# Kernel tuning notes

Hardware: AMD Instinct MI355X
Metric: run time of the kernel (lower is better)

Reference implementation:

```python
import jax, jax.numpy as jnp
import numpy as np

N = 1_000_000
SIZES = (64, 32, 16)
N_REGIONS = 1000
N_CLUSTERS = 16
N_CELLS = 100_000


def setup_inputs() -> dict:
    key = jax.random.key(0)
    ks = jax.random.split(key, 16)
    inp = {}
    for i, s in enumerate(SIZES):
        inp[f"bincounts_{i}"] = jax.random.randint(ks[i], (N, s), 0, 5, dtype=jnp.int32)
    inp["global_binixs"] = jax.random.randint(ks[3], (N, 3), 0, N_REGIONS, dtype=jnp.int32)
    inp["binixs"] = jax.random.randint(ks[4], (N, 3), 0, 16, dtype=jnp.int32)  # < min(SIZES)
    inp["labels"] = jax.random.randint(ks[5], (N_CELLS,), 0, N_CLUSTERS, dtype=jnp.int32)
    inp["local_cell_ix"] = jax.random.randint(ks[6], (N,), 0, N_CELLS, dtype=jnp.int32)
    for i, s in enumerate(SIZES):
        inp[f"baseline_{i}"] = jax.random.normal(ks[7 + i], (N_REGIONS, s), dtype=jnp.float32)
        inp[f"diff_{i}"] = jax.random.normal(ks[10 + i], (N_CLUSTERS,), dtype=jnp.float32)
    return inp


def reference(bincounts_0, bincounts_1, bincounts_2, global_binixs, binixs,
              labels, local_cell_ix, baseline_0, baseline_1, baseline_2,
              diff_0, diff_1, diff_2):
    # cluster label per fragment (int, constant)
    frag_labels = labels[local_cell_ix]  # [N]
    bincounts = (bincounts_0, bincounts_1, bincounts_2)
    baselines = (baseline_0, baseline_1, baseline_2)
    diffs = (diff_0, diff_1, diff_2)
    logprob = jnp.zeros((bincounts_0.shape[0],), dtype=jnp.float32)
    for i in range(3):
        bc, bw, dw = bincounts[i], baselines[i], diffs[i]
        S = bw.shape[1]
        # fragment_embedding (indicator) * differential scalar + baseline row
        dvals = dw[frag_labels]  # [N]
        uh = (bc > 1).astype(jnp.float32) * dvals[:, None] + bw[global_binixs[:, i]]  # [N, S]
        logh = jax.nn.log_softmax(uh, axis=1) + jnp.log(jnp.float32(S))
        logprob = logprob + jnp.take_along_axis(logh, binixs[:, i:i + 1], axis=1)[:, 0]
    return logprob
```

## Files before the change

kernel.cpp:

```cpp
#include <hip/hip_runtime.h>

#define LOG64f 4.1588830833596715f
#define LOG32f 3.4657359027997265f
#define LOG16f 2.7725887222397810f


__device__ __forceinline__ void expsum4(const int4 c, const float4 w, const float dv,
                                        const int b, const int sub, float& s, float& ub)
{
    const float u0 = (c.x > 1 ? dv : 0.f) + w.x;
    const float u1 = (c.y > 1 ? dv : 0.f) + w.y;
    const float u2 = (c.z > 1 ? dv : 0.f) + w.z;
    const float u3 = (c.w > 1 ? dv : 0.f) + w.w;
    s  = (__expf(u0) + __expf(u1)) + (__expf(u2) + __expf(u3));
    ub = 0.f;
    if (sub == (b >> 2)) {
        const int r = b & 3;
        ub = r == 0 ? u0 : r == 1 ? u1 : r == 2 ? u2 : u3;
    }
}

__device__ __forceinline__ float chunk16(
    const int lane,
    const int4 c00, const int4 c01, const int4 c02, const int4 c03,
    const int4 c10, const int4 c11, const int4 c20,
    const float dva, const float dvb, const float dvc,
    const int g0v, const int g1v, const int g2v,
    const int b0v, const int b1v, const int b2v,
    const float* __restrict__ bw0, const float* __restrict__ bw1,
    const float* __restrict__ bw2)
{
    const int fl = lane & 15;
    const int s16 = lane >> 4, s8 = lane >> 3, s4 = lane >> 2;
    const int f00 = s16, f01 = 4 + s16, f02 = 8 + s16, f03 = 12 + s16;
    const int f10 = s8,  f11 = 8 + s8;
    const int f20 = s4;
    const int sub0 = lane & 15, sub1 = lane & 7, sub2 = lane & 3;

    const float dv00 = __shfl(dva, f00), dv01 = __shfl(dva, f01),
                dv02 = __shfl(dva, f02), dv03 = __shfl(dva, f03);
    const int   g00  = __shfl(g0v, f00), g01  = __shfl(g0v, f01),
                g02  = __shfl(g0v, f02), g03  = __shfl(g0v, f03);
    const int   b00  = __shfl(b0v, f00), b01  = __shfl(b0v, f01),
                b02  = __shfl(b0v, f02), b03  = __shfl(b0v, f03);
    const float dv10 = __shfl(dvb, f10), dv11 = __shfl(dvb, f11);
    const int   g10  = __shfl(g1v, f10), g11  = __shfl(g1v, f11);
    const int   b10  = __shfl(b1v, f10), b11  = __shfl(b1v, f11);
    const float dv20 = __shfl(dvc, f20);
    const int   g20  = __shfl(g2v, f20);
    const int   b20  = __shfl(b2v, f20);

    const float4 w00 = ((const float4*)(bw0 + (size_t)g00 * 64))[sub0];
    const float4 w01 = ((const float4*)(bw0 + (size_t)g01 * 64))[sub0];
    const float4 w02 = ((const float4*)(bw0 + (size_t)g02 * 64))[sub0];
    const float4 w03 = ((const float4*)(bw0 + (size_t)g03 * 64))[sub0];
    const float4 w10 = ((const float4*)(bw1 + (size_t)g10 * 32))[sub1];
    const float4 w11 = ((const float4*)(bw1 + (size_t)g11 * 32))[sub1];
    const float4 w20 = ((const float4*)(bw2 + (size_t)g20 * 16))[sub2];

    float s00, u00, s01, u01, s02, u02, s03, u03;
    expsum4(c00, w00, dv00, b00, sub0, s00, u00);
    expsum4(c01, w01, dv01, b01, sub0, s01, u01);
    expsum4(c02, w02, dv02, b02, sub0, s02, u02);
    expsum4(c03, w03, dv03, b03, sub0, s03, u03);
    #pragma unroll
    for (int off = 1; off <= 8; off <<= 1) {
        s00 += __shfl_xor(s00, off); s01 += __shfl_xor(s01, off);
        s02 += __shfl_xor(s02, off); s03 += __shfl_xor(s03, off);
    }
    float s10, u10, s11, u11;
    expsum4(c10, w10, dv10, b10, sub1, s10, u10);
    expsum4(c11, w11, dv11, b11, sub1, s11, u11);
    #pragma unroll
    for (int off = 1; off <= 4; off <<= 1) {
        s10 += __shfl_xor(s10, off); s11 += __shfl_xor(s11, off);
    }
    float s20, u20;
    expsum4(c20, w20, dv20, b20, sub2, s20, u20);
    s20 += __shfl_xor(s20, 1); s20 += __shfl_xor(s20, 2);

    const int  src0 = (fl & 3) << 4;
    const float m00 = __shfl(s00, src0), m01 = __shfl(s01, src0),
                m02 = __shfl(s02, src0), m03 = __shfl(s03, src0);
    const int j0 = fl >> 2;
    const float S0 = j0 == 0 ? m00 : j0 == 1 ? m01 : j0 == 2 ? m02 : m03;
    const int  h0 = src0 + (b0v >> 2);
    const float x00 = __shfl(u00, h0), x01 = __shfl(u01, h0),
                x02 = __shfl(u02, h0), x03 = __shfl(u03, h0);
    const float U0 = j0 == 0 ? x00 : j0 == 1 ? x01 : j0 == 2 ? x02 : x03;

    const int  src1 = (fl & 7) << 3;
    const float m10 = __shfl(s10, src1), m11 = __shfl(s11, src1);
    const float S1 = (fl >> 3) == 0 ? m10 : m11;
    const int  h1 = src1 + (b1v >> 2);
    const float x10 = __shfl(u10, h1), x11 = __shfl(u11, h1);
    const float U1 = (fl >> 3) == 0 ? x10 : x11;

    const float S2 = __shfl(s20, fl << 2);
    const float U2 = __shfl(u20, (fl << 2) + (b2v >> 2));

    return (U0 - __logf(S0) + LOG64f) +
           (U1 - __logf(S1) + LOG32f) +
           (U2 - __logf(S2) + LOG16f);
}

__global__ __launch_bounds__(256) void frag_pos_dist_kernel(
    const int* __restrict__ bc0, const int* __restrict__ bc1, const int* __restrict__ bc2,
    const int* __restrict__ gix, const int* __restrict__ bix,
    const int* __restrict__ labels, const int* __restrict__ lci,
    const float* __restrict__ bw0, const float* __restrict__ d0,
    const float* __restrict__ bw1, const float* __restrict__ d1,
    const float* __restrict__ bw2, const float* __restrict__ d2,
    float* __restrict__ out, int N)
{
    const int lane = threadIdx.x & 63;
    const int wid  = blockIdx.x * (blockDim.x >> 6) + (threadIdx.x >> 6);
    const int base = wid * 32;
    if (base >= N) return;
    const int fl = lane & 15;
    const int s16 = lane >> 4, s8 = lane >> 3, s4 = lane >> 2;
    const int sub0 = lane & 15, sub1 = lane & 7, sub2 = lane & 3;
    const int NM1 = N - 1;

    const int nA00 = min(base +      s16, NM1), nA01 = min(base +  4 + s16, NM1),
              nA02 = min(base +  8 + s16, NM1), nA03 = min(base + 12 + s16, NM1);
    const int nA10 = min(base +       s8, NM1), nA11 = min(base +  8 +  s8, NM1);
    const int nA20 = min(base +       s4, NM1);
    const int nB00 = min(base + 16 + s16, NM1), nB01 = min(base + 20 + s16, NM1),
              nB02 = min(base + 24 + s16, NM1), nB03 = min(base + 28 + s16, NM1);
    const int nB10 = min(base + 16 +  s8, NM1), nB11 = min(base + 24 +  s8, NM1);
    const int nB20 = min(base + 16 +  s4, NM1);

    const int4 cA00 = ((const int4*)(bc0 + (size_t)nA00 * 64))[sub0];
    const int4 cA01 = ((const int4*)(bc0 + (size_t)nA01 * 64))[sub0];
    const int4 cA02 = ((const int4*)(bc0 + (size_t)nA02 * 64))[sub0];
    const int4 cA03 = ((const int4*)(bc0 + (size_t)nA03 * 64))[sub0];
    const int4 cA10 = ((const int4*)(bc1 + (size_t)nA10 * 32))[sub1];
    const int4 cA11 = ((const int4*)(bc1 + (size_t)nA11 * 32))[sub1];
    const int4 cA20 = ((const int4*)(bc2 + (size_t)nA20 * 16))[sub2];
    const int4 cB00 = ((const int4*)(bc0 + (size_t)nB00 * 64))[sub0];
    const int4 cB01 = ((const int4*)(bc0 + (size_t)nB01 * 64))[sub0];
    const int4 cB02 = ((const int4*)(bc0 + (size_t)nB02 * 64))[sub0];
    const int4 cB03 = ((const int4*)(bc0 + (size_t)nB03 * 64))[sub0];
    const int4 cB10 = ((const int4*)(bc1 + (size_t)nB10 * 32))[sub1];
    const int4 cB11 = ((const int4*)(bc1 + (size_t)nB11 * 32))[sub1];
    const int4 cB20 = ((const int4*)(bc2 + (size_t)nB20 * 16))[sub2];

    const int nfA = min(base + fl, NM1);
    const int nfB = min(base + 16 + fl, NM1);
    const int cellA = lci[nfA];
    const int cellB = lci[nfB];
    const int labA  = labels[cellA];
    const int labB  = labels[cellB];
    const float dvaA = d0[labA], dvbA = d1[labA], dvcA = d2[labA];
    const float dvaB = d0[labB], dvbB = d1[labB], dvcB = d2[labB];
    const int g0A = gix[3 * nfA + 0], g1A = gix[3 * nfA + 1], g2A = gix[3 * nfA + 2];
    const int g0B = gix[3 * nfB + 0], g1B = gix[3 * nfB + 1], g2B = gix[3 * nfB + 2];
    const int b0A = bix[3 * nfA + 0], b1A = bix[3 * nfA + 1], b2A = bix[3 * nfA + 2];
    const int b0B = bix[3 * nfB + 0], b1B = bix[3 * nfB + 1], b2B = bix[3 * nfB + 2];

    const float accA = chunk16(lane, cA00, cA01, cA02, cA03, cA10, cA11, cA20,
                               dvaA, dvbA, dvcA, g0A, g1A, g2A, b0A, b1A, b2A,
                               bw0, bw1, bw2);
    const float accB = chunk16(lane, cB00, cB01, cB02, cB03, cB10, cB11, cB20,
                               dvaB, dvbB, dvcB, g0B, g1B, g2B, b0B, b1B, b2B,
                               bw0, bw1, bw2);

    if (lane < 32) {
        const int n = base + lane;
        if (n < N) out[n] = (lane < 16) ? accA : accB;
    }
}

extern "C" void kernel_launch(void* const* d_in, const int* in_sizes, int n_in,
                              void* d_out, int out_size, void* d_ws, size_t ws_size,
                              hipStream_t stream) {
    const int* bc0    = (const int*)d_in[0];
    const int* bc1    = (const int*)d_in[1];
    const int* bc2    = (const int*)d_in[2];
    const int* gix    = (const int*)d_in[3];
    const int* bixp   = (const int*)d_in[4];
    const int* labels = (const int*)d_in[5];
    const int* lci    = (const int*)d_in[6];
    const float* bw0  = (const float*)d_in[7];
    const float* dv0  = (const float*)d_in[8];
    const float* bw1  = (const float*)d_in[9];
    const float* dv1  = (const float*)d_in[10];
    const float* bw2  = (const float*)d_in[11];
    const float* dv2  = (const float*)d_in[12];
    float* out = (float*)d_out;

    const int N = in_sizes[6];
    const int threads = 256;
    const int fragsPerBlock = 128;
    const int blocks = (N + fragsPerBlock - 1) / fragsPerBlock;

    frag_pos_dist_kernel<<<blocks, threads, 0, stream>>>(
        bc0, bc1, bc2, gix, bixp, labels, lci,
        bw0, dv0, bw1, dv1, bw2, dv2, out, N);
}
```

Measured before the change: 104.1 us.

## Use persistent grid-stride waves with double-buffered register prefetch of fragment groups

```diff
diff --git a/kernel.cpp b/kernel.cpp
--- a/kernel.cpp
+++ b/kernel.cpp
@@ -4,6 +4,12 @@
 #define LOG32f 3.4657359027997265f
 #define LOG16f 2.7725887222397810f
 
+
+struct Frag {
+    int4 c00, c01, c02, c03, c10, c11, c20;
+    float dva, dvb, dvc;
+    int g0, g1, g2, b0, b1, b2;
+};
 
 __device__ __forceinline__ void expsum4(const int4 c, const float4 w, const float dv,
                                         const int b, const int sub, float& s, float& ub)
@@ -20,15 +26,42 @@
     }
 }
 
-__device__ __forceinline__ float chunk16(
-    const int lane,
-    const int4 c00, const int4 c01, const int4 c02, const int4 c03,
-    const int4 c10, const int4 c11, const int4 c20,
-    const float dva, const float dvb, const float dvc,
-    const int g0v, const int g1v, const int g2v,
-    const int b0v, const int b1v, const int b2v,
+__device__ __forceinline__ void load_group(
+    Frag& F, const int base, const int NM1, const int lane,
+    const int* __restrict__ bc0, const int* __restrict__ bc1, const int* __restrict__ bc2,
+    const int* __restrict__ gix, const int* __restrict__ bix,
+    const int* __restrict__ labels, const int* __restrict__ lci,
+    const float* __restrict__ d0, const float* __restrict__ d1, const float* __restrict__ d2)
+{
+    const int s16 = lane >> 4, s8 = lane >> 3, s4 = lane >> 2;
+    const int sub0 = lane & 15, sub1 = lane & 7, sub2 = lane & 3;
+    const int fl = lane & 15;
+
+    const int n00 = min(base +      s16, NM1), n01 = min(base +  4 + s16, NM1),
+              n02 = min(base +  8 + s16, NM1), n03 = min(base + 12 + s16, NM1);
+    const int n10 = min(base +       s8, NM1), n11 = min(base +  8 +  s8, NM1);
+    const int n20 = min(base +       s4, NM1);
+
+    F.c00 = ((const int4*)(bc0 + (size_t)n00 * 64))[sub0];
+    F.c01 = ((const int4*)(bc0 + (size_t)n01 * 64))[sub0];
+    F.c02 = ((const int4*)(bc0 + (size_t)n02 * 64))[sub0];
+    F.c03 = ((const int4*)(bc0 + (size_t)n03 * 64))[sub0];
+    F.c10 = ((const int4*)(bc1 + (size_t)n10 * 32))[sub1];
+    F.c11 = ((const int4*)(bc1 + (size_t)n11 * 32))[sub1];
+    F.c20 = ((const int4*)(bc2 + (size_t)n20 * 16))[sub2];
+
+    const int nf = min(base + fl, NM1);
+    const int cell = lci[nf];
+    F.g0 = gix[3 * nf + 0]; F.g1 = gix[3 * nf + 1]; F.g2 = gix[3 * nf + 2];
+    F.b0 = bix[3 * nf + 0]; F.b1 = bix[3 * nf + 1]; F.b2 = bix[3 * nf + 2];
+    const int lab = labels[cell];
+    F.dva = d0[lab]; F.dvb = d1[lab]; F.dvc = d2[lab];
+}
+
+__device__ __forceinline__ void compute_store(
+    const Frag& F, const int lane, const int base, const int N,
     const float* __restrict__ bw0, const float* __restrict__ bw1,
-    const float* __restrict__ bw2)
+    const float* __restrict__ bw2, float* __restrict__ out)
 {
     const int fl = lane & 15;
     const int s16 = lane >> 4, s8 = lane >> 3, s4 = lane >> 2;
@@ -37,18 +70,18 @@
     const int f20 = s4;
     const int sub0 = lane & 15, sub1 = lane & 7, sub2 = lane & 3;
 
-    const float dv00 = __shfl(dva, f00), dv01 = __shfl(dva, f01),
-                dv02 = __shfl(dva, f02), dv03 = __shfl(dva, f03);
-    const int   g00  = __shfl(g0v, f00), g01  = __shfl(g0v, f01),
-                g02  = __shfl(g0v, f02), g03  = __shfl(g0v, f03);
-    const int   b00  = __shfl(b0v, f00), b01  = __shfl(b0v, f01),
-                b02  = __shfl(b0v, f02), b03  = __shfl(b0v, f03);
-    const float dv10 = __shfl(dvb, f10), dv11 = __shfl(dvb, f11);
-    const int   g10  = __shfl(g1v, f10), g11  = __shfl(g1v, f11);
-    const int   b10  = __shfl(b1v, f10), b11  = __shfl(b1v, f11);
-    const float dv20 = __shfl(dvc, f20);
-    const int   g20  = __shfl(g2v, f20);
-    const int   b20  = __shfl(b2v, f20);
+    const float dv00 = __shfl(F.dva, f00), dv01 = __shfl(F.dva, f01),
+                dv02 = __shfl(F.dva, f02), dv03 = __shfl(F.dva, f03);
+    const int   g00  = __shfl(F.g0, f00), g01 = __shfl(F.g0, f01),
+                g02  = __shfl(F.g0, f02), g03 = __shfl(F.g0, f03);
+    const int   b00  = __shfl(F.b0, f00), b01 = __shfl(F.b0, f01),
+                b02  = __shfl(F.b0, f02), b03 = __shfl(F.b0, f03);
+    const float dv10 = __shfl(F.dvb, f10), dv11 = __shfl(F.dvb, f11);
+    const int   g10  = __shfl(F.g1, f10), g11 = __shfl(F.g1, f11);
+    const int   b10  = __shfl(F.b1, f10), b11 = __shfl(F.b1, f11);
+    const float dv20 = __shfl(F.dvc, f20);
+    const int   g20  = __shfl(F.g2, f20);
+    const int   b20  = __shfl(F.b2, f20);
 
     const float4 w00 = ((const float4*)(bw0 + (size_t)g00 * 64))[sub0];
     const float4 w01 = ((const float4*)(bw0 + (size_t)g01 * 64))[sub0];
@@ -59,24 +92,24 @@
     const float4 w20 = ((const float4*)(bw2 + (size_t)g20 * 16))[sub2];
 
     float s00, u00, s01, u01, s02, u02, s03, u03;
-    expsum4(c00, w00, dv00, b00, sub0, s00, u00);
-    expsum4(c01, w01, dv01, b01, sub0, s01, u01);
-    expsum4(c02, w02, dv02, b02, sub0, s02, u02);
-    expsum4(c03, w03, dv03, b03, sub0, s03, u03);
+    expsum4(F.c00, w00, dv00, b00, sub0, s00, u00);
+    expsum4(F.c01, w01, dv01, b01, sub0, s01, u01);
+    expsum4(F.c02, w02, dv02, b02, sub0, s02, u02);
+    expsum4(F.c03, w03, dv03, b03, sub0, s03, u03);
     #pragma unroll
     for (int off = 1; off <= 8; off <<= 1) {
         s00 += __shfl_xor(s00, off); s01 += __shfl_xor(s01, off);
         s02 += __shfl_xor(s02, off); s03 += __shfl_xor(s03, off);
     }
     float s10, u10, s11, u11;
-    expsum4(c10, w10, dv10, b10, sub1, s10, u10);
-    expsum4(c11, w11, dv11, b11, sub1, s11, u11);
+    expsum4(F.c10, w10, dv10, b10, sub1, s10, u10);
+    expsum4(F.c11, w11, dv11, b11, sub1, s11, u11);
     #pragma unroll
     for (int off = 1; off <= 4; off <<= 1) {
         s10 += __shfl_xor(s10, off); s11 += __shfl_xor(s11, off);
     }
     float s20, u20;
-    expsum4(c20, w20, dv20, b20, sub2, s20, u20);
+    expsum4(F.c20, w20, dv20, b20, sub2, s20, u20);
     s20 += __shfl_xor(s20, 1); s20 += __shfl_xor(s20, 2);
 
     const int  src0 = (fl & 3) << 4;
@@ -84,7 +117,7 @@
                 m02 = __shfl(s02, src0), m03 = __shfl(s03, src0);
     const int j0 = fl >> 2;
     const float S0 = j0 == 0 ? m00 : j0 == 1 ? m01 : j0 == 2 ? m02 : m03;
-    const int  h0 = src0 + (b0v >> 2);
+    const int  h0 = src0 + (F.b0 >> 2);
     const float x00 = __shfl(u00, h0), x01 = __shfl(u01, h0),
                 x02 = __shfl(u02, h0), x03 = __shfl(u03, h0);
     const float U0 = j0 == 0 ? x00 : j0 == 1 ? x01 : j0 == 2 ? x02 : x03;
@@ -92,16 +125,21 @@
     const int  src1 = (fl & 7) << 3;
     const float m10 = __shfl(s10, src1), m11 = __shfl(s11, src1);
     const float S1 = (fl >> 3) == 0 ? m10 : m11;
-    const int  h1 = src1 + (b1v >> 2);
+    const int  h1 = src1 + (F.b1 >> 2);
     const float x10 = __shfl(u10, h1), x11 = __shfl(u11, h1);
     const float U1 = (fl >> 3) == 0 ? x10 : x11;
 
     const float S2 = __shfl(s20, fl << 2);
-    const float U2 = __shfl(u20, (fl << 2) + (b2v >> 2));
-
-    return (U0 - __logf(S0) + LOG64f) +
-           (U1 - __logf(S1) + LOG32f) +
-           (U2 - __logf(S2) + LOG16f);
+    const float U2 = __shfl(u20, (fl << 2) + (F.b2 >> 2));
+
+    const float acc = (U0 - __logf(S0) + LOG64f) +
+                      (U1 - __logf(S1) + LOG32f) +
+                      (U2 - __logf(S2) + LOG16f);
+
+    if (lane < 16) {
+        const int n = base + lane;
+        if (n < N) out[n] = acc;
+    }
 }
 
 __global__ __launch_bounds__(256) void frag_pos_dist_kernel(
@@ -113,62 +151,35 @@
     const float* __restrict__ bw2, const float* __restrict__ d2,
     float* __restrict__ out, int N)
 {
-    const int lane = threadIdx.x & 63;
-    const int wid  = blockIdx.x * (blockDim.x >> 6) + (threadIdx.x >> 6);
-    const int base = wid * 32;
-    if (base >= N) return;
-    const int fl = lane & 15;
-    const int s16 = lane >> 4, s8 = lane >> 3, s4 = lane >> 2;
-    const int sub0 = lane & 15, sub1 = lane & 7, sub2 = lane & 3;
+    const int lane   = threadIdx.x & 63;
+    const int nWaves = gridDim.x * (blockDim.x >> 6);
+    const int wid    = blockIdx.x * (blockDim.x >> 6) + (threadIdx.x >> 6);
+    const int nGroups = (N + 15) >> 4;
     const int NM1 = N - 1;
 
-    const int nA00 = min(base +      s16, NM1), nA01 = min(base +  4 + s16, NM1),
-              nA02 = min(base +  8 + s16, NM1), nA03 = min(base + 12 + s16, NM1);
-    const int nA10 = min(base +       s8, NM1), nA11 = min(base +  8 +  s8, NM1);
-    const int nA20 = min(base +       s4, NM1);
-    const int nB00 = min(base + 16 + s16, NM1), nB01 = min(base + 20 + s16, NM1),
-              nB02 = min(base + 24 + s16, NM1), nB03 = min(base + 28 + s16, NM1);
-    const int nB10 = min(base + 16 +  s8, NM1), nB11 = min(base + 24 +  s8, NM1);
-    const int nB20 = min(base + 16 +  s4, NM1);
-
-    const int4 cA00 = ((const int4*)(bc0 + (size_t)nA00 * 64))[sub0];
-    const int4 cA01 = ((const int4*)(bc0 + (size_t)nA01 * 64))[sub0];
-    const int4 cA02 = ((const int4*)(bc0 + (size_t)nA02 * 64))[sub0];
-    const int4 cA03 = ((const int4*)(bc0 + (size_t)nA03 * 64))[sub0];
-    const int4 cA10 = ((const int4*)(bc1 + (size_t)nA10 * 32))[sub1];
-    const int4 cA11 = ((const int4*)(bc1 + (size_t)nA11 * 32))[sub1];
-    const int4 cA20 = ((const int4*)(bc2 + (size_t)nA20 * 16))[sub2];
-    const int4 cB00 = ((const int4*)(bc0 + (size_t)nB00 * 64))[sub0];
-    const int4 cB01 = ((const int4*)(bc0 + (size_t)nB01 * 64))[sub0];
-    const int4 cB02 = ((const int4*)(bc0 + (size_t)nB02 * 64))[sub0];
-    const int4 cB03 = ((const int4*)(bc0 + (size_t)nB03 * 64))[sub0];
-    const int4 cB10 = ((const int4*)(bc1 + (size_t)nB10 * 32))[sub1];
-    const int4 cB11 = ((const int4*)(bc1 + (size_t)nB11 * 32))[sub1];
-    const int4 cB20 = ((const int4*)(bc2 + (size_t)nB20 * 16))[sub2];
-
-    const int nfA = min(base + fl, NM1);
-    const int nfB = min(base + 16 + fl, NM1);
-    const int cellA = lci[nfA];
-    const int cellB = lci[nfB];
-    const int labA  = labels[cellA];
-    const int labB  = labels[cellB];
-    const float dvaA = d0[labA], dvbA = d1[labA], dvcA = d2[labA];
-    const float dvaB = d0[labB], dvbB = d1[labB], dvcB = d2[labB];
-    const int g0A = gix[3 * nfA + 0], g1A = gix[3 * nfA + 1], g2A = gix[3 * nfA + 2];
-    const int g0B = gix[3 * nfB + 0], g1B = gix[3 * nfB + 1], g2B = gix[3 * nfB + 2];
-    const int b0A = bix[3 * nfA + 0], b1A = bix[3 * nfA + 1], b2A = bix[3 * nfA + 2];
-    const int b0B = bix[3 * nfB + 0], b1B = bix[3 * nfB + 1], b2B = bix[3 * nfB + 2];
-
-    const float accA = chunk16(lane, cA00, cA01, cA02, cA03, cA10, cA11, cA20,
-                               dvaA, dvbA, dvcA, g0A, g1A, g2A, b0A, b1A, b2A,
-                               bw0, bw1, bw2);
-    const float accB = chunk16(lane, cB00, cB01, cB02, cB03, cB10, cB11, cB20,
-                               dvaB, dvbB, dvcB, g0B, g1B, g2B, b0B, b1B, b2B,
-                               bw0, bw1, bw2);
-
-    if (lane < 32) {
-        const int n = base + lane;
-        if (n < N) out[n] = (lane < 16) ? accA : accB;
+    int g = wid;
+    if (g >= nGroups) return;
+
+    Frag A, B;
+    load_group(A, g * 16, NM1, lane, bc0, bc1, bc2, gix, bix, labels, lci, d0, d1, d2);
+    int gn = g + nWaves;
+    bool moreB = gn < nGroups;
+    if (moreB)
+        load_group(B, gn * 16, NM1, lane, bc0, bc1, bc2, gix, bix, labels, lci, d0, d1, d2);
+
+    for (;;) {
+        compute_store(A, lane, g * 16, N, bw0, bw1, bw2, out);
+        if (!moreB) return;
+        g = gn; gn = g + nWaves;
+        const bool moreA = gn < nGroups;
+        if (moreA)
+            load_group(A, gn * 16, NM1, lane, bc0, bc1, bc2, gix, bix, labels, lci, d0, d1, d2);
+        compute_store(B, lane, g * 16, N, bw0, bw1, bw2, out);
+        if (!moreA) return;
+        g = gn; gn = g + nWaves;
+        moreB = gn < nGroups;
+        if (moreB)
+            load_group(B, gn * 16, NM1, lane, bc0, bc1, bc2, gix, bix, labels, lci, d0, d1, d2);
     }
 }
 
@@ -191,11 +202,13 @@
     float* out = (float*)d_out;
 
     const int N = in_sizes[6];
-    const int threads = 256;
-    const int fragsPerBlock = 128;
-    const int blocks = (N + fragsPerBlock - 1) / fragsPerBlock;
-
-    frag_pos_dist_kernel<<<blocks, threads, 0, stream>>>(
+    const int nGroups = (N + 15) / 16;
+    const int wavesPerBlock = 4;
+    const int maxBlocks = 2048;
+    int blocks = (nGroups + wavesPerBlock - 1) / wavesPerBlock;
+    if (blocks > maxBlocks) blocks = maxBlocks;
+
+    frag_pos_dist_kernel<<<blocks, 256, 0, stream>>>(
         bc0, bc1, bc2, gix, bixp, labels, lci,
         bw0, dv0, bw1, dv1, bw2, dv2, out, N);
 }
```

Measured after the change: 121.1 us. +16.4%, slower.

## Add prepass packing per-fragment indices into int2 records and halve frags per wave

Applied to the files above, without the earlier changes.

```diff
diff --git a/kernel.cpp b/kernel.cpp
--- a/kernel.cpp
+++ b/kernel.cpp
@@ -4,6 +4,22 @@
 #define LOG32f 3.4657359027997265f
 #define LOG16f 2.7725887222397810f
 
+
+__global__ __launch_bounds__(256) void prepass_kernel(
+    const int* __restrict__ gix, const int* __restrict__ bix,
+    const int* __restrict__ labels, const int* __restrict__ lci,
+    int2* __restrict__ rec, int N)
+{
+    const int n = blockIdx.x * blockDim.x + threadIdx.x;
+    if (n >= N) return;
+    const int lab = labels[lci[n]];
+    const int g0 = gix[3 * n + 0], g1 = gix[3 * n + 1], g2 = gix[3 * n + 2];
+    const int b0 = bix[3 * n + 0], b1 = bix[3 * n + 1], b2 = bix[3 * n + 2];
+    int2 w;
+    w.x = lab | (g0 << 4) | (b0 << 14) | (g1 << 18);
+    w.y = b1 | (g2 << 4) | (b2 << 14);
+    rec[n] = w;
+}
 
 __device__ __forceinline__ void expsum4(const int4 c, const float4 w, const float dv,
                                         const int b, const int sub, float& s, float& ub)
@@ -20,35 +36,72 @@
     }
 }
 
-__device__ __forceinline__ float chunk16(
-    const int lane,
-    const int4 c00, const int4 c01, const int4 c02, const int4 c03,
-    const int4 c10, const int4 c11, const int4 c20,
-    const float dva, const float dvb, const float dvc,
-    const int g0v, const int g1v, const int g2v,
-    const int b0v, const int b1v, const int b2v,
-    const float* __restrict__ bw0, const float* __restrict__ bw1,
-    const float* __restrict__ bw2)
+__global__ __launch_bounds__(256) void frag_pos_dist_kernel(
+    const int* __restrict__ bc0, const int* __restrict__ bc1, const int* __restrict__ bc2,
+    const int* __restrict__ gix, const int* __restrict__ bix,
+    const int* __restrict__ labels, const int* __restrict__ lci,
+    const float* __restrict__ bw0, const float* __restrict__ d0,
+    const float* __restrict__ bw1, const float* __restrict__ d1,
+    const float* __restrict__ bw2, const float* __restrict__ d2,
+    const int2* __restrict__ rec,
+    float* __restrict__ out, int N)
 {
+    const int lane = threadIdx.x & 63;
+    const int wid  = blockIdx.x * (blockDim.x >> 6) + (threadIdx.x >> 6);
+    const int base = wid * 16;
+    if (base >= N) return;
     const int fl = lane & 15;
+    const int NM1 = N - 1;
+
     const int s16 = lane >> 4, s8 = lane >> 3, s4 = lane >> 2;
     const int f00 = s16, f01 = 4 + s16, f02 = 8 + s16, f03 = 12 + s16;
     const int f10 = s8,  f11 = 8 + s8;
     const int f20 = s4;
     const int sub0 = lane & 15, sub1 = lane & 7, sub2 = lane & 3;
 
-    const float dv00 = __shfl(dva, f00), dv01 = __shfl(dva, f01),
-                dv02 = __shfl(dva, f02), dv03 = __shfl(dva, f03);
-    const int   g00  = __shfl(g0v, f00), g01  = __shfl(g0v, f01),
-                g02  = __shfl(g0v, f02), g03  = __shfl(g0v, f03);
-    const int   b00  = __shfl(b0v, f00), b01  = __shfl(b0v, f01),
-                b02  = __shfl(b0v, f02), b03  = __shfl(b0v, f03);
-    const float dv10 = __shfl(dvb, f10), dv11 = __shfl(dvb, f11);
-    const int   g10  = __shfl(g1v, f10), g11  = __shfl(g1v, f11);
-    const int   b10  = __shfl(b1v, f10), b11  = __shfl(b1v, f11);
-    const float dv20 = __shfl(dvc, f20);
-    const int   g20  = __shfl(g2v, f20);
-    const int   b20  = __shfl(b2v, f20);
+    const int n00 = min(base +      s16, NM1), n01 = min(base +  4 + s16, NM1),
+              n02 = min(base +  8 + s16, NM1), n03 = min(base + 12 + s16, NM1);
+    const int n10 = min(base +       s8, NM1), n11 = min(base +  8 +  s8, NM1);
+    const int n20 = min(base +       s4, NM1);
+
+    const int4 c00 = ((const int4*)(bc0 + (size_t)n00 * 64))[sub0];
+    const int4 c01 = ((const int4*)(bc0 + (size_t)n01 * 64))[sub0];
+    const int4 c02 = ((const int4*)(bc0 + (size_t)n02 * 64))[sub0];
+    const int4 c03 = ((const int4*)(bc0 + (size_t)n03 * 64))[sub0];
+    const int4 c10 = ((const int4*)(bc1 + (size_t)n10 * 32))[sub1];
+    const int4 c11 = ((const int4*)(bc1 + (size_t)n11 * 32))[sub1];
+    const int4 c20 = ((const int4*)(bc2 + (size_t)n20 * 16))[sub2];
+
+    const int nf = min(base + fl, NM1);
+    int w0, w1;
+    if (rec) {
+        const int2 pw = rec[nf];
+        w0 = pw.x; w1 = pw.y;
+    } else {
+        const int lab = labels[lci[nf]];
+        const int g0 = gix[3 * nf + 0], g1 = gix[3 * nf + 1], g2 = gix[3 * nf + 2];
+        const int b0 = bix[3 * nf + 0], b1 = bix[3 * nf + 1], b2 = bix[3 * nf + 2];
+        w0 = lab | (g0 << 4) | (b0 << 14) | (g1 << 18);
+        w1 = b1 | (g2 << 4) | (b2 << 14);
+    }
+
+    const int W000 = __shfl(w0, f00), W001 = __shfl(w0, f01),
+              W002 = __shfl(w0, f02), W003 = __shfl(w0, f03);
+    const int W010 = __shfl(w0, f10), W110 = __shfl(w1, f10);
+    const int W011 = __shfl(w0, f11), W111 = __shfl(w1, f11);
+    const int W020 = __shfl(w0, f20), W120 = __shfl(w1, f20);
+
+    const float dv00 = d0[W000 & 15]; const int g00 = (W000 >> 4) & 1023, b00 = (W000 >> 14) & 15;
+    const float dv01 = d0[W001 & 15]; const int g01 = (W001 >> 4) & 1023, b01 = (W001 >> 14) & 15;
+    const float dv02 = d0[W002 & 15]; const int g02 = (W002 >> 4) & 1023, b02 = (W002 >> 14) & 15;
+    const float dv03 = d0[W003 & 15]; const int g03 = (W003 >> 4) & 1023, b03 = (W003 >> 14) & 15;
+    const float dv10 = d1[W010 & 15]; const int g10 = (W010 >> 18) & 1023, b10 = W110 & 15;
+    const float dv11 = d1[W011 & 15]; const int g11 = (W011 >> 18) & 1023, b11 = W111 & 15;
+    const float dv20 = d2[W020 & 15]; const int g20 = (W120 >> 4) & 1023, b20 = (W120 >> 14) & 15;
+
+    const int b0o = (w0 >> 14) & 15;
+    const int b1o = w1 & 15;
+    const int b2o = (w1 >> 14) & 15;
 
     const float4 w00 = ((const float4*)(bw0 + (size_t)g00 * 64))[sub0];
     const float4 w01 = ((const float4*)(bw0 + (size_t)g01 * 64))[sub0];
@@ -84,7 +137,7 @@
                 m02 = __shfl(s02, src0), m03 = __shfl(s03, src0);
     const int j0 = fl >> 2;
     const float S0 = j0 == 0 ? m00 : j0 == 1 ? m01 : j0 == 2 ? m02 : m03;
-    const int  h0 = src0 + (b0v >> 2);
+    const int  h0 = src0 + (b0o >> 2);
     const float x00 = __shfl(u00, h0), x01 = __shfl(u01, h0),
                 x02 = __shfl(u02, h0), x03 = __shfl(u03, h0);
     const float U0 = j0 == 0 ? x00 : j0 == 1 ? x01 : j0 == 2 ? x02 : x03;
@@ -92,83 +145,20 @@
     const int  src1 = (fl & 7) << 3;
     const float m10 = __shfl(s10, src1), m11 = __shfl(s11, src1);
     const float S1 = (fl >> 3) == 0 ? m10 : m11;
-    const int  h1 = src1 + (b1v >> 2);
+    const int  h1 = src1 + (b1o >> 2);
     const float x10 = __shfl(u10, h1), x11 = __shfl(u11, h1);
     const float U1 = (fl >> 3) == 0 ? x10 : x11;
 
     const float S2 = __shfl(s20, fl << 2);
-    const float U2 = __shfl(u20, (fl << 2) + (b2v >> 2));
+    const float U2 = __shfl(u20, (fl << 2) + (b2o >> 2));
 
-    return (U0 - __logf(S0) + LOG64f) +
-           (U1 - __logf(S1) + LOG32f) +
-           (U2 - __logf(S2) + LOG16f);
-}
+    const float acc = (U0 - __logf(S0) + LOG64f) +
+                      (U1 - __logf(S1) + LOG32f) +
+                      (U2 - __logf(S2) + LOG16f);
 
-__global__ __launch_bounds__(256) void frag_pos_dist_kernel(
-    const int* __restrict__ bc0, const int* __restrict__ bc1, const int* __restrict__ bc2,
-    const int* __restrict__ gix, const int* __restrict__ bix,
-    const int* __restrict__ labels, const int* __restrict__ lci,
-    const float* __restrict__ bw0, const float* __restrict__ d0,
-    const float* __restrict__ bw1, const float* __restrict__ d1,
-    const float* __restrict__ bw2, const float* __restrict__ d2,
-    float* __restrict__ out, int N)
-{
-    const int lane = threadIdx.x & 63;
-    const int wid  = blockIdx.x * (blockDim.x >> 6) + (threadIdx.x >> 6);
-    const int base = wid * 32;
-    if (base >= N) return;
-    const int fl = lane & 15;
-    const int s16 = lane >> 4, s8 = lane >> 3, s4 = lane >> 2;
-    const int sub0 = lane & 15, sub1 = lane & 7, sub2 = lane & 3;
-    const int NM1 = N - 1;
-
-    const int nA00 = min(base +      s16, NM1), nA01 = min(base +  4 + s16, NM1),
-              nA02 = min(base +  8 + s16, NM1), nA03 = min(base + 12 + s16, NM1);
-    const int nA10 = min(base +       s8, NM1), nA11 = min(base +  8 +  s8, NM1);
-    const int nA20 = min(base +       s4, NM1);
-    const int nB00 = min(base + 16 + s16, NM1), nB01 = min(base + 20 + s16, NM1),
-              nB02 = min(base + 24 + s16, NM1), nB03 = min(base + 28 + s16, NM1);
-    const int nB10 = min(base + 16 +  s8, NM1), nB11 = min(base + 24 +  s8, NM1);
-    const int nB20 = min(base + 16 +  s4, NM1);
-
-    const int4 cA00 = ((const int4*)(bc0 + (size_t)nA00 * 64))[sub0];
-    const int4 cA01 = ((const int4*)(bc0 + (size_t)nA01 * 64))[sub0];
-    const int4 cA02 = ((const int4*)(bc0 + (size_t)nA02 * 64))[sub0];
-    const int4 cA03 = ((const int4*)(bc0 + (size_t)nA03 * 64))[sub0];
-    const int4 cA10 = ((const int4*)(bc1 + (size_t)nA10 * 32))[sub1];
-    const int4 cA11 = ((const int4*)(bc1 + (size_t)nA11 * 32))[sub1];
-    const int4 cA20 = ((const int4*)(bc2 + (size_t)nA20 * 16))[sub2];
-    const int4 cB00 = ((const int4*)(bc0 + (size_t)nB00 * 64))[sub0];
-    const int4 cB01 = ((const int4*)(bc0 + (size_t)nB01 * 64))[sub0];
-    const int4 cB02 = ((const int4*)(bc0 + (size_t)nB02 * 64))[sub0];
-    const int4 cB03 = ((const int4*)(bc0 + (size_t)nB03 * 64))[sub0];
-    const int4 cB10 = ((const int4*)(bc1 + (size_t)nB10 * 32))[sub1];
-    const int4 cB11 = ((const int4*)(bc1 + (size_t)nB11 * 32))[sub1];
-    const int4 cB20 = ((const int4*)(bc2 + (size_t)nB20 * 16))[sub2];
-
-    const int nfA = min(base + fl, NM1);
-    const int nfB = min(base + 16 + fl, NM1);
-    const int cellA = lci[nfA];
-    const int cellB = lci[nfB];
-    const int labA  = labels[cellA];
-    const int labB  = labels[cellB];
-    const float dvaA = d0[labA], dvbA = d1[labA], dvcA = d2[labA];
-    const float dvaB = d0[labB], dvbB = d1[labB], dvcB = d2[labB];
-    const int g0A = gix[3 * nfA + 0], g1A = gix[3 * nfA + 1], g2A = gix[3 * nfA + 2];
-    const int g0B = gix[3 * nfB + 0], g1B = gix[3 * nfB + 1], g2B = gix[3 * nfB + 2];
-    const int b0A = bix[3 * nfA + 0], b1A = bix[3 * nfA + 1], b2A = bix[3 * nfA + 2];
-    const int b0B = bix[3 * nfB + 0], b1B = bix[3 * nfB + 1], b2B = bix[3 * nfB + 2];
-
-    const float accA = chunk16(lane, cA00, cA01, cA02, cA03, cA10, cA11, cA20,
-                               dvaA, dvbA, dvcA, g0A, g1A, g2A, b0A, b1A, b2A,
-                               bw0, bw1, bw2);
-    const float accB = chunk16(lane, cB00, cB01, cB02, cB03, cB10, cB11, cB20,
-                               dvaB, dvbB, dvcB, g0B, g1B, g2B, b0B, b1B, b2B,
-                               bw0, bw1, bw2);
-
-    if (lane < 32) {
+    if (lane < 16) {
         const int n = base + lane;
-        if (n < N) out[n] = (lane < 16) ? accA : accB;
+        if (n < N) out[n] = acc;
     }
 }
 
@@ -191,11 +181,17 @@
     float* out = (float*)d_out;
 
     const int N = in_sizes[6];
-    const int threads = 256;
-    const int fragsPerBlock = 128;
+
+    int2* rec = nullptr;
+    if (ws_size >= (size_t)N * sizeof(int2)) {
+        rec = (int2*)d_ws;
+        prepass_kernel<<<(N + 255) / 256, 256, 0, stream>>>(
+            gix, bixp, labels, lci, rec, N);
+    }
+
+    const int fragsPerBlock = 64;
     const int blocks = (N + fragsPerBlock - 1) / fragsPerBlock;
-
-    frag_pos_dist_kernel<<<blocks, threads, 0, stream>>>(
+    frag_pos_dist_kernel<<<blocks, 256, 0, stream>>>(
         bc0, bc1, bc2, gix, bixp, labels, lci,
-        bw0, dv0, bw1, dv1, bw2, dv2, out, N);
+        bw0, dv0, bw1, dv1, bw2, dv2, rec, out, N);
 }
```

Result: no change. 104.5 us (+0.4%).
